# Kernel optimization log

Hardware: AMD Instinct MI355X
Metric: run time of the kernel (lower is better)

Reference implementation:

```python
import jax, jax.numpy as jnp
import numpy as np

D_MODEL = 512
NUM_HEADS = 8
HEAD_DIM = D_MODEL // NUM_HEADS
NEG_INF = -1e9


def setup_inputs() -> dict:
    key = jax.random.key(0)
    ks = jax.random.split(key, 12)
    B, S = 4, 2048
    std = 1.0 / np.sqrt(D_MODEL)
    inp = {
        "query": jax.random.normal(ks[0], (B, S, D_MODEL), jnp.float32),
        "key": jax.random.normal(ks[1], (B, S, D_MODEL), jnp.float32),
        "value": jax.random.normal(ks[2], (B, S, D_MODEL), jnp.float32),
        "mask": jax.random.randint(ks[3], (B, 1, S, S), 0, 2, jnp.int32),
        "Wq": jax.random.normal(ks[4], (D_MODEL, D_MODEL), jnp.float32) * std,
        "bq": jnp.zeros((D_MODEL,), jnp.float32),
        "Wk": jax.random.normal(ks[5], (D_MODEL, D_MODEL), jnp.float32) * std,
        "bk": jnp.zeros((D_MODEL,), jnp.float32),
        "Wv": jax.random.normal(ks[6], (D_MODEL, D_MODEL), jnp.float32) * std,
        "bv": jnp.zeros((D_MODEL,), jnp.float32),
        "Wo": jax.random.normal(ks[7], (D_MODEL, D_MODEL), jnp.float32) * std,
        "bo": jnp.zeros((D_MODEL,), jnp.float32),
    }
    return inp


def _split_heads(x):
    B, S, _ = x.shape
    return x.reshape(B, S, NUM_HEADS, HEAD_DIM).transpose(0, 2, 1, 3)  # [B,H,S,Dh]


def reference(query, key, value, mask, Wq, bq, Wk, bk, Wv, bv, Wo, bo):
    B, S, _ = query.shape
    q = _split_heads(query @ Wq + bq)
    k = _split_heads(key @ Wk + bk)
    v = _split_heads(value @ Wv + bv)
    # scores: [B,H,S,S]
    scores = jnp.einsum("bhqd,bhkd->bhqk", q, k) / jnp.sqrt(jnp.float32(HEAD_DIM))
    scores = jnp.where(mask == 0, jnp.float32(NEG_INF), scores)
    attn = jax.nn.softmax(scores, axis=-1)  # dropout p=0 -> identity
    out = jnp.einsum("bhqk,bhkd->bhqd", attn, v)
    out = out.transpose(0, 2, 1, 3).reshape(B, S, D_MODEL)
    return out @ Wo + bo
```

## Files before the change

kernel.cpp:

```cpp
#include <hip/hip_runtime.h>
#include <hip/hip_bf16.h>

typedef unsigned short u16;
typedef __attribute__((ext_vector_type(4))) float f32x4;
typedef __attribute__((ext_vector_type(16))) float f32x16;
typedef __attribute__((ext_vector_type(8))) short s16x8;
typedef __attribute__((ext_vector_type(4))) unsigned short u16x4;

__device__ __forceinline__ u16 f2bf(float f) {
    union { float f; unsigned u; } v; v.f = f;
    unsigned r = v.u + 0x7fffu + ((v.u >> 16) & 1u);
    return (u16)(r >> 16);
}
__device__ __forceinline__ u16 f2bfh(float f) {
    __hip_bfloat16 h = __float2bfloat16(f);
    return *reinterpret_cast<u16*>(&h);
}
__device__ __forceinline__ float fexp2(float x) {
#if __has_builtin(__builtin_amdgcn_exp2f)
    return __builtin_amdgcn_exp2f(x);
#else
    return exp2f(x);
#endif
}
__device__ __forceinline__ void gload16(const void* g, void* lds_uniform) {
    __builtin_amdgcn_global_load_lds(
        (const __attribute__((address_space(1))) void*)g,
        (__attribute__((address_space(3))) void*)lds_uniform, 16, 0, 0);
}
__device__ __forceinline__ f32x4 mfma16(s16x8 a, s16x8 b, f32x4 c) {
    return __builtin_amdgcn_mfma_f32_16x16x32_bf16(a, b, c, 0, 0, 0);
}
__device__ __forceinline__ f32x16 mfma32(s16x8 a, s16x8 b, f32x16 c) {
    return __builtin_amdgcn_mfma_f32_32x32x16_bf16(a, b, c, 0, 0, 0);
}

__global__ void prep(const float4* __restrict__ q, const float4* __restrict__ k,
                     const float4* __restrict__ v, u16x4* __restrict__ qkv,
                     const float* __restrict__ Wq, const float* __restrict__ Wk,
                     const float* __restrict__ Wv, const float* __restrict__ Wo,
                     u16* __restrict__ WqT, u16* __restrict__ WkT,
                     u16* __restrict__ WvT, u16* __restrict__ WoT,
                     const int* __restrict__ mask, unsigned* __restrict__ bits) {
    __shared__ float tile[32][33];
    const int bid = blockIdx.x, tid = threadIdx.x;
    if (bid < 12288) {
        int i = bid * 256 + tid;
        int sel = i >> 20, j = i & 0xFFFFF;
        const float4* in = (sel == 0) ? q : (sel == 1) ? k : v;
        float4 f = in[j];
        u16x4 o;
        o[0] = f2bf(f.x); o[1] = f2bf(f.y); o[2] = f2bf(f.z); o[3] = f2bf(f.w);
        qkv[i] = o;
    } else if (bid < 13312) {
        int idx = bid - 12288;
        int bz = idx >> 8, rem = idx & 255, by = rem >> 4, bx = rem & 15;
        const float* W; u16* T;
        switch (bz) {
            case 0: W = Wq; T = WqT; break;
            case 1: W = Wk; T = WkT; break;
            case 2: W = Wv; T = WvT; break;
            default: W = Wo; T = WoT; break;
        }
        const int tx = tid & 31, ty = tid >> 5;
        const int k0 = by * 32, n0 = bx * 32;
#pragma unroll
        for (int r = 0; r < 32; r += 8) tile[ty + r][tx] = W[(k0 + ty + r) * 512 + n0 + tx];
        __syncthreads();
#pragma unroll
        for (int r = 0; r < 32; r += 8) T[(n0 + ty + r) * 512 + k0 + tx] = f2bf(tile[tx][ty + r]);
    } else {
        int i = (bid - 13312) * 256 + tid;
        int m = mask[i];
        unsigned long long bal = __ballot(m != 0);
        if ((tid & 63) == 0) {
            uint2 w2; w2.x = (unsigned)bal; w2.y = (unsigned)(bal >> 32);
            *(uint2*)&bits[i >> 5] = w2;
        }
    }
}

template <int BM, int BIAS_ROW, int OUT_F32>
__global__ __launch_bounds__(256, 4) void gemm_bt(
    const u16* __restrict__ A, const u16* __restrict__ Bt0, const u16* __restrict__ Bt1,
    const float* __restrict__ bias0, const float* __restrict__ bias1,
    void* __restrict__ Cout, int M, int N, int K, int ysplit,
    float scale0, float scale1) {
    constexpr int MR = BM / 32;
    const u16* Bt = (blockIdx.y < (unsigned)ysplit) ? Bt0 : Bt1;
    const float* bias = (blockIdx.y < (unsigned)ysplit) ? bias0 : bias1;
    const float scale = (blockIdx.y < (unsigned)ysplit) ? scale0 : scale1;
    __shared__ u16 As[BM * 64];
    __shared__ u16 Bs[64 * 64];
    const int t = threadIdx.x, l = t & 63, w = t >> 6;
    const int lr = l & 15, lg = l >> 4;
    const int m0 = blockIdx.y * BM, n0 = blockIdx.x * 64;
    const int wr = w >> 1, wc = w & 1;
    f32x4 acc[MR][2] = {};
    const int tr = t >> 3, tc8 = (t & 7) * 8;

    for (int kk = 0; kk < K; kk += 64) {
        __syncthreads();
#pragma unroll
        for (int i = 0; i < MR; ++i)
            gload16(A + (m0 + i * 32 + tr) * K + kk + tc8, As + i * 2048 + w * 512);
#pragma unroll
        for (int i = 0; i < 2; ++i)
            gload16(Bt + (n0 + i * 32 + tr) * K + kk + tc8, Bs + i * 2048 + w * 512);
        __syncthreads();
        s16x8 af[MR][2], bfr[2][2];
#pragma unroll
        for (int m = 0; m < MR; ++m)
#pragma unroll
            for (int kh = 0; kh < 2; ++kh)
                af[m][kh] = *(const s16x8*)&As[(wr * (BM / 2) + m * 16 + lr) * 64 + kh * 32 + lg * 8];
#pragma unroll
        for (int n = 0; n < 2; ++n)
#pragma unroll
            for (int kh = 0; kh < 2; ++kh)
                bfr[n][kh] = *(const s16x8*)&Bs[(wc * 32 + n * 16 + lr) * 64 + kh * 32 + lg * 8];
#pragma unroll
        for (int m = 0; m < MR; ++m)
#pragma unroll
            for (int n = 0; n < 2; ++n)
#pragma unroll
                for (int kh = 0; kh < 2; ++kh)
                    acc[m][n] = mfma16(af[m][kh], bfr[n][kh], acc[m][n]);
    }

#pragma unroll
    for (int n = 0; n < 2; ++n) {
        const int cg = n0 + wc * 32 + n * 16 + lr;
        const float bcol = BIAS_ROW ? 0.f : bias[cg];
#pragma unroll
        for (int m = 0; m < MR; ++m) {
            const int rbase = m0 + wr * (BM / 2) + m * 16 + lg * 4;
#pragma unroll
            for (int j = 0; j < 4; ++j) {
                const int rg = rbase + j;
                float val = (acc[m][n][j] + (BIAS_ROW ? bias[rg] : bcol)) * scale;
                if (OUT_F32) ((float*)Cout)[(size_t)rg * N + cg] = val;
                else         ((u16*)Cout)[(size_t)rg * N + cg] = f2bf(val);
            }
        }
    }
}

__global__ __launch_bounds__(256, 2) void attn_fwd(
    const u16* __restrict__ Qp, const u16* __restrict__ Kp,
    const u16* __restrict__ Vt, const unsigned* __restrict__ mbits,
    u16* __restrict__ AO) {
    constexpr int S = 2048;
    const int qt = blockIdx.x, bh = blockIdx.y;
    const int b = bh >> 3, h = bh & 7;
    const int t = threadIdx.x, l = t & 63, w = t >> 6;
    const int lq = l & 31, hi = l >> 5;
    const int hi8 = hi * 8, hi4 = hi * 4;

    __shared__ u16 Ks[2][64 * 64];
    __shared__ u16 Vs[2][64 * 64];

    const int q0w = qt * 128 + w * 32;
    const int bS = b * S;

    s16x8 qf[4];
#pragma unroll
    for (int ds = 0; ds < 4; ++ds)
        qf[ds] = *(const s16x8*)&Qp[(bS + q0w + lq) * 512 + h * 64 + ds * 16 + hi8];

    f32x16 po[2];
#pragma unroll
    for (int r = 0; r < 16; ++r) { po[0][r] = 0.f; po[1][r] = 0.f; }
    float lrun = 0.f;

    const int kc0 = t, kc1 = 256 + t;
    const int krow0 = kc0 >> 3, kcol0 = ((kc0 & 7) ^ (krow0 & 7)) * 8;
    const int krow1 = kc1 >> 3, kcol1 = ((kc1 & 7) ^ (krow1 & 7)) * 8;

#define STAGE(nb, kt0)                                                              \
    do {                                                                            \
        gload16(&Kp[(bS + (kt0) + krow0) * 512 + h * 64 + kcol0], &Ks[nb][w * 512]);\
        gload16(&Kp[(bS + (kt0) + krow1) * 512 + h * 64 + kcol1], &Ks[nb][2048 + w * 512]);\
        gload16(&Vt[(h * 64 + krow0) * (4 * S) + bS + (kt0) + kcol0], &Vs[nb][w * 512]);\
        gload16(&Vt[(h * 64 + krow1) * (4 * S) + bS + (kt0) + kcol1], &Vs[nb][2048 + w * 512]);\
    } while (0)

    STAGE(0, 0);
    uint2 mwv = *(const uint2*)&mbits[(bS + q0w + lq) * 64];
    uint2 mwn = mwv;

    for (int it = 0; it < 32; ++it) {
        const int cur = it & 1;
        __syncthreads();
        if (it + 1 < 32) {
            STAGE(cur ^ 1, (it + 1) * 64);
            mwn = *(const uint2*)&mbits[(bS + q0w + lq) * 64 + ((it + 1) << 1)];
        }
        const u16* Kc = Ks[cur];
        const u16* Vc = Vs[cur];

        s16x8 bq[4];
#pragma unroll
        for (int kt_t = 0; kt_t < 2; ++kt_t) {
            f32x16 sc;
#pragma unroll
            for (int r = 0; r < 16; ++r) sc[r] = 0.f;
            __builtin_amdgcn_s_setprio(1);
#pragma unroll
            for (int ds = 0; ds < 4; ++ds) {
                const int row = kt_t * 32 + lq;
                const int byte = (row * 128 + ds * 32 + hi * 16) ^ ((row & 7) << 4);
                s16x8 ka = *(const s16x8*)((const char*)Kc + byte);
                sc = mfma32(ka, qf[ds], sc);
            }
            __builtin_amdgcn_s_setprio(0);

            const unsigned w32 = kt_t ? mwv.y : mwv.x;
            float p[16];
            float ps = 0.f;
#pragma unroll
            for (int r = 0; r < 16; ++r) {
                const int shift = (r & 3) + 8 * (r >> 2);
                const float s = ((w32 >> (shift + hi4)) & 1u) ? sc[r] : -1e9f;
                p[r] = fexp2(s);
                ps += p[r];
            }
            lrun += ps;

            unsigned pk[8];
#pragma unroll
            for (int i = 0; i < 8; ++i) {
                unsigned v;
                asm("v_cvt_pk_bf16_f32 %0, %1, %2"
                    : "=v"(v) : "v"(p[2 * i]), "v"(p[2 * i + 1]));
                pk[i] = v;
            }
            asm("v_permlane32_swap_b32 %0, %1" : "+v"(pk[0]), "+v"(pk[2]));
            asm("v_permlane32_swap_b32 %0, %1" : "+v"(pk[1]), "+v"(pk[3]));
            asm("v_permlane32_swap_b32 %0, %1" : "+v"(pk[4]), "+v"(pk[6]));
            asm("v_permlane32_swap_b32 %0, %1" : "+v"(pk[5]), "+v"(pk[7]));
            union BQ { unsigned u[4]; s16x8 v; } b0, b1;
            b0.u[0] = pk[0]; b0.u[1] = pk[1]; b0.u[2] = pk[2]; b0.u[3] = pk[3];
            b1.u[0] = pk[4]; b1.u[1] = pk[5]; b1.u[2] = pk[6]; b1.u[3] = pk[7];
            bq[kt_t * 2]     = b0.v;
            bq[kt_t * 2 + 1] = b1.v;
        }

        __builtin_amdgcn_s_setprio(1);
#pragma unroll
        for (int dt = 0; dt < 2; ++dt)
#pragma unroll
            for (int ks = 0; ks < 4; ++ks) {
                const int row = dt * 32 + lq;
                const int byte = (row * 128 + ks * 32 + hi * 16) ^ ((row & 7) << 4);
                s16x8 va = *(const s16x8*)((const char*)Vc + byte);
                po[dt] = mfma32(va, bq[ks], po[dt]);
            }
        __builtin_amdgcn_s_setprio(0);

        mwv = mwn;
    }
#undef STAGE

    lrun += __shfl_xor(lrun, 32);
    const float inv = 1.f / lrun;
    const int orow = (bS + q0w + lq) * 512 + h * 64;
#pragma unroll
    for (int dt = 0; dt < 2; ++dt)
#pragma unroll
        for (int r = 0; r < 16; r += 2) {
            const int d = dt * 32 + (r & 3) + 8 * (r >> 2) + hi4;
            const unsigned lo = f2bfh(po[dt][r] * inv);
            const unsigned hh = f2bfh(po[dt][r + 1] * inv);
            *(unsigned*)&AO[orow + d] = lo | (hh << 16);
        }
}

extern "C" void kernel_launch(void* const* d_in, const int* in_sizes, int n_in,
                              void* d_out, int out_size, void* d_ws, size_t ws_size,
                              hipStream_t stream) {
    (void)in_sizes; (void)n_in; (void)out_size; (void)ws_size;
    const float* query = (const float*)d_in[0];
    const float* key   = (const float*)d_in[1];
    const float* value = (const float*)d_in[2];
    const int*   mask  = (const int*)d_in[3];
    const float* Wq = (const float*)d_in[4];
    const float* bq = (const float*)d_in[5];
    const float* Wk = (const float*)d_in[6];
    const float* bk = (const float*)d_in[7];
    const float* Wv = (const float*)d_in[8];
    const float* bv = (const float*)d_in[9];
    const float* Wo = (const float*)d_in[10];
    const float* bo = (const float*)d_in[11];

    char* ws = (char*)d_ws;
    const size_t MB = 1ull << 20;
    u16* qb  = (u16*)(ws);
    u16* vb  = (u16*)(ws + 16 * MB);
    u16* WqT = (u16*)(ws + 24 * MB);
    u16* WkT = (u16*)(ws + 24 * MB + 512 * 1024);
    u16* WvT = (u16*)(ws + 25 * MB);
    u16* WoT = (u16*)(ws + 25 * MB + 512 * 1024);
    unsigned* mb = (unsigned*)(ws + 26 * MB);
    u16* Qp = (u16*)(ws + 28 * MB);
    u16* Vt = (u16*)(ws + 44 * MB);
    u16* AO = (u16*)(ws + 52 * MB);

    prep<<<78848, 256, 0, stream>>>((const float4*)query, (const float4*)key,
                                    (const float4*)value, (u16x4*)qb,
                                    Wq, Wk, Wv, Wo, WqT, WkT, WvT, WoT, mask, mb);

    gemm_bt<128, 0, 0><<<dim3(8, 128), 256, 0, stream>>>(
        qb, WqT, WkT, bq, bk, Qp, 16384, 512, 512, 64, 0.18033688f, 1.0f);
    gemm_bt<64, 1, 0><<<dim3(128, 8), 256, 0, stream>>>(
        WvT, vb, vb, bv, bv, Vt, 512, 8192, 512, 999, 1.0f, 1.0f);

    attn_fwd<<<dim3(16, 32), 256, 0, stream>>>(Qp, Qp + 8192 * 512, Vt, mb, AO);

    gemm_bt<64, 0, 1><<<dim3(8, 128), 256, 0, stream>>>(
        AO, WoT, WoT, bo, bo, (float*)d_out, 8192, 512, 512, 999, 1.0f, 1.0f);
}
```

Before: 150.7 us.

## Split attention over two key halves and merge partials in a combine kernel

The attention kernel now launches a third grid dimension that gives each block half of the key range. Each block writes a bf16 partial output, normalised by its own denominator, and stores that row-sum to a workspace. A new combine kernel blends the two partials, weighting each by its share of the total denominator. Launch bounds go from 2 to 4 blocks per CU, raising occupancy and doubling the block count so the low-occupancy attention grid fills the GPU better. The cost is an extra pass over partial outputs, bf16 rounding of the partials, and register pressure from the tighter launch bounds.

New measurement: 149.3 us. No clear change (-1.0%).

```diff
diff --git a/kernel.cpp b/kernel.cpp
--- a/kernel.cpp
+++ b/kernel.cpp
@@ -15,6 +15,10 @@
 __device__ __forceinline__ u16 f2bfh(float f) {
     __hip_bfloat16 h = __float2bfloat16(f);
     return *reinterpret_cast<u16*>(&h);
+}
+__device__ __forceinline__ float bf2f(u16 h) {
+    union { unsigned u; float f; } v; v.u = ((unsigned)h) << 16;
+    return v.f;
 }
 __device__ __forceinline__ float fexp2(float x) {
 #if __has_builtin(__builtin_amdgcn_exp2f)
@@ -146,12 +150,13 @@
     }
 }
 
-__global__ __launch_bounds__(256, 2) void attn_fwd(
+__global__ __launch_bounds__(256, 4) void attn_fwd(
     const u16* __restrict__ Qp, const u16* __restrict__ Kp,
     const u16* __restrict__ Vt, const unsigned* __restrict__ mbits,
-    u16* __restrict__ AO) {
+    u16* __restrict__ ppo, float* __restrict__ lws) {
     constexpr int S = 2048;
     const int qt = blockIdx.x, bh = blockIdx.y;
+    const int kbase = (int)blockIdx.z << 10;
     const int b = bh >> 3, h = bh & 7;
     const int t = threadIdx.x, l = t & 63, w = t >> 6;
     const int lq = l & 31, hi = l >> 5;
@@ -185,16 +190,17 @@
         gload16(&Vt[(h * 64 + krow1) * (4 * S) + bS + (kt0) + kcol1], &Vs[nb][2048 + w * 512]);\
     } while (0)
 
-    STAGE(0, 0);
-    uint2 mwv = *(const uint2*)&mbits[(bS + q0w + lq) * 64];
+    const int mrow = (bS + q0w + lq) * 64 + (kbase >> 5);
+    STAGE(0, kbase);
+    uint2 mwv = *(const uint2*)&mbits[mrow];
     uint2 mwn = mwv;
 
-    for (int it = 0; it < 32; ++it) {
+    for (int it = 0; it < 16; ++it) {
         const int cur = it & 1;
         __syncthreads();
-        if (it + 1 < 32) {
-            STAGE(cur ^ 1, (it + 1) * 64);
-            mwn = *(const uint2*)&mbits[(bS + q0w + lq) * 64 + ((it + 1) << 1)];
+        if (it + 1 < 16) {
+            STAGE(cur ^ 1, kbase + (it + 1) * 64);
+            mwn = *(const uint2*)&mbits[mrow + ((it + 1) << 1)];
         }
         const u16* Kc = Ks[cur];
         const u16* Vc = Vs[cur];
@@ -264,6 +270,7 @@
 
     lrun += __shfl_xor(lrun, 32);
     const float inv = 1.f / lrun;
+    u16* pp = ppo + (size_t)blockIdx.z * 4194304;
     const int orow = (bS + q0w + lq) * 512 + h * 64;
 #pragma unroll
     for (int dt = 0; dt < 2; ++dt)
@@ -272,8 +279,26 @@
             const int d = dt * 32 + (r & 3) + 8 * (r >> 2) + hi4;
             const unsigned lo = f2bfh(po[dt][r] * inv);
             const unsigned hh = f2bfh(po[dt][r + 1] * inv);
-            *(unsigned*)&AO[orow + d] = lo | (hh << 16);
-        }
+            *(unsigned*)&pp[orow + d] = lo | (hh << 16);
+        }
+    if (hi == 0) lws[blockIdx.z * 65536 + bh * 2048 + q0w + lq] = lrun;
+}
+
+__global__ __launch_bounds__(256) void combine(const u16* __restrict__ po,
+                                               const float* __restrict__ lw,
+                                               u16* __restrict__ AO) {
+    const int i = (blockIdx.x * 256 + threadIdx.x) * 8;
+    const int row = i >> 9, col = i & 511;
+    const int lidx = ((row >> 11) * 8 + (col >> 6)) * 2048 + (row & 2047);
+    const float la = lw[lidx], lb = lw[65536 + lidx];
+    const float wa = la / (la + lb), wb = 1.f - wa;
+    s16x8 a = *(const s16x8*)&po[i];
+    s16x8 c = *(const s16x8*)&po[4194304 + i];
+    s16x8 o;
+#pragma unroll
+    for (int j = 0; j < 8; ++j)
+        o[j] = (short)f2bfh(bf2f((u16)a[j]) * wa + bf2f((u16)c[j]) * wb);
+    *(s16x8*)&AO[i] = o;
 }
 
 extern "C" void kernel_launch(void* const* d_in, const int* in_sizes, int n_in,
@@ -305,6 +330,8 @@
     u16* Qp = (u16*)(ws + 28 * MB);
     u16* Vt = (u16*)(ws + 44 * MB);
     u16* AO = (u16*)(ws + 52 * MB);
+    u16* ppo = (u16*)(ws);
+    float* lws = (float*)(ws + 17 * MB);
 
     prep<<<78848, 256, 0, stream>>>((const float4*)query, (const float4*)key,
                                     (const float4*)value, (u16x4*)qb,
@@ -315,7 +342,8 @@
     gemm_bt<64, 1, 0><<<dim3(128, 8), 256, 0, stream>>>(
         WvT, vb, vb, bv, bv, Vt, 512, 8192, 512, 999, 1.0f, 1.0f);
 
-    attn_fwd<<<dim3(16, 32), 256, 0, stream>>>(Qp, Qp + 8192 * 512, Vt, mb, AO);
+    attn_fwd<<<dim3(16, 32, 2), 256, 0, stream>>>(Qp, Qp + 8192 * 512, Vt, mb, ppo, lws);
+    combine<<<2048, 256, 0, stream>>>(ppo, lws, AO);
 
     gemm_bt<64, 0, 1><<<dim3(8, 128), 256, 0, stream>>>(
         AO, WoT, WoT, bo, bo, (float*)d_out, 8192, 512, 512, 999, 1.0f, 1.0f);
```
